# Optimization experiments

Hardware: AMD Instinct MI355X
Metric: run time of the kernel (lower is better)

The kernel has to match this reference:

```python
import jax, jax.numpy as jnp
import numpy as np

B = 2; C = 3; IMG = 224; P = 16
DIM = 256; DEPTH = 2; HEADS = 4; DH = 64; MLP = 1024; NCLS = 1000
GRID = IMG // P            # 14
NPATCH = GRID * GRID       # 196
T = NPATCH + 1             # 197 (cls token)
PATCH_DIM = C * P * P      # 768


def _ln(x, g, b):
    m = x.mean(-1, keepdims=True)
    v = ((x - m) ** 2).mean(-1, keepdims=True)
    return (x - m) * jax.lax.rsqrt(v + 1e-5) * g + b


def _trittention(x, ln_g, ln_b, w_abcde, b_abcde, w_out, b_out):
    b, t, _ = x.shape
    xn = _ln(x, ln_g, ln_b)
    abcde = xn @ w_abcde + b_abcde                      # [b,t,5*H*DH]
    a, bb, c, d, e = jnp.split(abcde, 5, axis=-1)
    rs = lambda z: z.reshape(b, t, HEADS, DH)
    a, bb, c, d, e = map(rs, (a, bb, c, d, e))
    # cubic ternary scores: [b, h, q, s, t]
    s = jnp.einsum('bshd,bthd,bqhd->bhqst', a, bb, c) / DH
    p = jax.nn.softmax(s.reshape(b, HEADS, t, t * t), axis=-1)
    p = p.reshape(b, HEADS, t, t, t)
    z = jnp.einsum('bhqlr,blhd->bhqd', p, d) + jnp.einsum('bhqlr,brhd->bhqd', p, e)
    z = z.transpose(0, 2, 1, 3).reshape(b, t, HEADS * DH)
    return z @ w_out + b_out


def _ff(x, ln_g, ln_b, w1, b1, w2, b2):
    h = jax.nn.gelu(_ln(x, ln_g, ln_b) @ w1 + b1, approximate=False)
    return h @ w2 + b2


def setup_inputs() -> dict:
    key = jax.random.key(0)
    ks = jax.random.split(key, 10)
    s = 0.02
    d = {}
    d['img'] = jax.random.normal(ks[0], (B, C, IMG, IMG), jnp.float32)
    d['patch_ln1_g'] = jnp.ones((PATCH_DIM,), jnp.float32)
    d['patch_ln1_b'] = jnp.zeros((PATCH_DIM,), jnp.float32)
    d['patch_w'] = jax.random.normal(ks[1], (PATCH_DIM, DIM), jnp.float32) * s
    d['patch_b'] = jnp.zeros((DIM,), jnp.float32)
    d['patch_ln2_g'] = jnp.ones((DIM,), jnp.float32)
    d['patch_ln2_b'] = jnp.zeros((DIM,), jnp.float32)
    d['pos_emb'] = jax.random.normal(ks[2], (1, T, DIM), jnp.float32) * s
    d['cls_token'] = jax.random.normal(ks[3], (1, 1, DIM), jnp.float32) * s
    d['attn_ln_g'] = jnp.ones((DEPTH, DIM), jnp.float32)
    d['attn_ln_b'] = jnp.zeros((DEPTH, DIM), jnp.float32)
    d['w_abcde'] = jax.random.normal(ks[4], (DEPTH, DIM, 5 * HEADS * DH), jnp.float32) * s
    d['b_abcde'] = jnp.zeros((DEPTH, 5 * HEADS * DH), jnp.float32)
    d['w_out'] = jax.random.normal(ks[5], (DEPTH, HEADS * DH, DIM), jnp.float32) * s
    d['b_out'] = jnp.zeros((DEPTH, DIM), jnp.float32)
    d['ff_ln_g'] = jnp.ones((DEPTH, DIM), jnp.float32)
    d['ff_ln_b'] = jnp.zeros((DEPTH, DIM), jnp.float32)
    d['ff_w1'] = jax.random.normal(ks[6], (DEPTH, DIM, MLP), jnp.float32) * s
    d['ff_b1'] = jnp.zeros((DEPTH, MLP), jnp.float32)
    d['ff_w2'] = jax.random.normal(ks[7], (DEPTH, MLP, DIM), jnp.float32) * s
    d['ff_b2'] = jnp.zeros((DEPTH, DIM), jnp.float32)
    d['final_ln_g'] = jnp.ones((DIM,), jnp.float32)
    d['final_ln_b'] = jnp.zeros((DIM,), jnp.float32)
    d['head_w'] = jax.random.normal(ks[8], (DIM, NCLS), jnp.float32) * s
    d['head_b'] = jnp.zeros((NCLS,), jnp.float32)
    return d


def reference(img, patch_ln1_g, patch_ln1_b, patch_w, patch_b, patch_ln2_g, patch_ln2_b,
              pos_emb, cls_token, attn_ln_g, attn_ln_b, w_abcde, b_abcde, w_out, b_out,
              ff_ln_g, ff_ln_b, ff_w1, ff_b1, ff_w2, ff_b2, final_ln_g, final_ln_b,
              head_w, head_b):
    b = img.shape[0]
    # Rearrange 'b c (h p1) (w p2) -> b (h w) (p1 p2 c)'
    x = img.reshape(b, C, GRID, P, GRID, P).transpose(0, 2, 4, 3, 5, 1)
    x = x.reshape(b, NPATCH, PATCH_DIM)
    x = _ln(x, patch_ln1_g, patch_ln1_b)
    x = x @ patch_w + patch_b
    x = _ln(x, patch_ln2_g, patch_ln2_b)
    cls = jnp.broadcast_to(cls_token, (b, 1, DIM))
    x = jnp.concatenate([cls, x], axis=1) + pos_emb
    for i in range(DEPTH):
        x = _trittention(x, attn_ln_g[i], attn_ln_b[i], w_abcde[i], b_abcde[i],
                         w_out[i], b_out[i]) + x
        x = _ff(x, ff_ln_g[i], ff_ln_b[i], ff_w1[i], ff_b1[i], ff_w2[i], ff_b2[i]) + x
    x = _ln(x, final_ln_g, final_ln_b)
    return x[:, 0] @ head_w + head_b
```

## Files before the change

kernel.cpp:

```cpp
#include <hip/hip_runtime.h>
#include <hip/hip_bf16.h>

#define BB 2
#define TT 197
#define TP 208
#define NT16 13
#define DIMM 256
#define HEADS_ 4
#define DH_ 64
#define ABCDE_N 1280
#define MLP_ 1024
#define NCLS_ 1000
#define PATCH_DIM_ 768

typedef __attribute__((ext_vector_type(8))) short short8_t;
typedef __attribute__((ext_vector_type(4))) float f32x4;

__device__ __forceinline__ float waveReduceSum(float v) {
#pragma unroll
    for (int off = 32; off > 0; off >>= 1) v += __shfl_xor(v, off, 64);
    return v;
}

__device__ __forceinline__ float rowReduceSum16(float v) {
    v += __uint_as_float(__builtin_amdgcn_update_dpp(
            0, __float_as_uint(v), 0x121, 0xF, 0xF, true));
    v += __uint_as_float(__builtin_amdgcn_update_dpp(
            0, __float_as_uint(v), 0x122, 0xF, 0xF, true));
    v += __uint_as_float(__builtin_amdgcn_update_dpp(
            0, __float_as_uint(v), 0x124, 0xF, 0xF, true));
    v += __uint_as_float(__builtin_amdgcn_update_dpp(
            0, __float_as_uint(v), 0x128, 0xF, 0xF, true));
    return v;
}

__device__ __forceinline__ unsigned short f2bf(float x) {
    unsigned int u = __float_as_uint(x);
    u += 0x7FFFu + ((u >> 16) & 1u);
    return (unsigned short)(u >> 16);
}

__device__ __forceinline__ float bf2f(unsigned short u) {
    return __uint_as_float(((unsigned int)u) << 16);
}

__global__ __launch_bounds__(256) void patch_embed_k(
    const float* __restrict__ img, const float* __restrict__ g1, const float* __restrict__ b1,
    const float* __restrict__ pw, const float* __restrict__ pb,
    const float* __restrict__ g2, const float* __restrict__ b2,
    const float* __restrict__ pos, const float* __restrict__ cls,
    float* __restrict__ xa)
{
    int tid = threadIdx.x;
    if (blockIdx.x == 98) {
        for (int b = 0; b < BB; b++)
            xa[(long)b * TT * DIMM + tid] = cls[tid] + pos[tid];
        return;
    }
    __shared__ __align__(16) float xs[4][PATCH_DIM_];
    __shared__ float red[8];
    int pr0 = blockIdx.x * 4;
    for (int r = 0; r < 4; r++) {
        int pr = pr0 + r;
        int b = pr / 196, patch = pr % 196;
        int gh = patch / 14, gw = patch % 14;
        for (int j = tid; j < PATCH_DIM_; j += 256) {
            int c = j % 3, p2 = (j / 3) % 16, p1 = j / 48;
            xs[r][j] = img[(((long)b * 3 + c) * 224 + gh * 16 + p1) * 224 + gw * 16 + p2];
        }
    }
    __syncthreads();
    int wv = tid >> 6, lane = tid & 63;
    {
        int r = wv;
        float s = 0.f, s2 = 0.f;
        for (int j = lane; j < PATCH_DIM_; j += 64) { float v = xs[r][j]; s += v; s2 += v * v; }
        s = waveReduceSum(s); s2 = waveReduceSum(s2);
        float m = s / PATCH_DIM_;
        float rs = rsqrtf(s2 / PATCH_DIM_ - m * m + 1e-5f);
        for (int j = lane; j < PATCH_DIM_; j += 64)
            xs[r][j] = (xs[r][j] - m) * rs * g1[j] + b1[j];
    }
    __syncthreads();
    float acc[4] = {0.f, 0.f, 0.f, 0.f};
    for (int k = 0; k < PATCH_DIM_; k += 4) {
        float w0 = pw[(k + 0) * DIMM + tid];
        float w1 = pw[(k + 1) * DIMM + tid];
        float w2 = pw[(k + 2) * DIMM + tid];
        float w3 = pw[(k + 3) * DIMM + tid];
#pragma unroll
        for (int r = 0; r < 4; r++) {
            float4 xv = *(const float4*)&xs[r][k];
            acc[r] = fmaf(xv.x, w0, fmaf(xv.y, w1, fmaf(xv.z, w2, fmaf(xv.w, w3, acc[r]))));
        }
    }
#pragma unroll
    for (int r = 0; r < 4; r++) acc[r] += pb[tid];
    for (int r = 0; r < 4; r++) {
        float s = waveReduceSum(acc[r]);
        float s2 = waveReduceSum(acc[r] * acc[r]);
        if (lane == 0) { red[wv * 2] = s; red[wv * 2 + 1] = s2; }
        __syncthreads();
        float S = red[0] + red[2] + red[4] + red[6];
        float S2 = red[1] + red[3] + red[5] + red[7];
        __syncthreads();
        float m = S / DIMM;
        float rs = rsqrtf(S2 / DIMM - m * m + 1e-5f);
        int pr = pr0 + r;
        int b = pr / 196, patch = pr % 196;
        float v = (acc[r] - m) * rs * g2[tid] + b2[tid] + pos[(1 + patch) * DIMM + tid];
        xa[((long)b * TT + 1 + patch) * DIMM + tid] = v;
    }
}

__global__ __launch_bounds__(512) void gemm_ksplit_k(
    const float* __restrict__ x, long x_stride, int M, int K, int N,
    const float* __restrict__ w, const float* __restrict__ bias,
    const float* __restrict__ res, float* __restrict__ out,
    const float* __restrict__ ln_g, const float* __restrict__ ln_b,
    int do_gelu)
{
    __shared__ __align__(16) float xs[4 * 1024];
    __shared__ float psum[8 * 4 * 64];
    int tid = threadIdx.x, lane = tid & 63, wv = tid >> 6;
    int row0 = blockIdx.y * 4, col0 = blockIdx.x * 64;

    for (int i = tid; i < 4 * K; i += 512) {
        int r = i / K, k = i - r * K;
        int row = row0 + r;
        xs[i] = (row < M) ? x[(long)row * x_stride + k] : 0.f;
    }
    __syncthreads();
    if (ln_g) {
        if (wv < 4) {
            float* xr = xs + wv * K;
            float s = 0.f, s2 = 0.f;
            for (int k = lane; k < K; k += 64) { float v = xr[k]; s += v; s2 += v * v; }
            s = waveReduceSum(s); s2 = waveReduceSum(s2);
            float m = s / K;
            float rs = rsqrtf(s2 / K - m * m + 1e-5f);
            for (int k = lane; k < K; k += 64)
                xr[k] = (xr[k] - m) * rs * ln_g[k] + ln_b[k];
        }
        __syncthreads();
    }

    int col = col0 + lane;
    float a0 = 0.f, a1 = 0.f, a2 = 0.f, a3 = 0.f;
    int kq = K >> 3;
    if (col < N) {
        const float* x0 = xs + wv * kq;
        const float* x1 = x0 + K;
        const float* x2 = x1 + K;
        const float* x3 = x2 + K;
        const float* wp = w + (long)(wv * kq) * N + col;
        long nl = N;
        for (int kk = 0; kk < kq; kk += 4) {
            float w0 = wp[0], w1 = wp[nl], w2 = wp[2 * nl], w3 = wp[3 * nl];
            wp += 4 * nl;
            float4 v0 = *(const float4*)(x0 + kk);
            float4 v1 = *(const float4*)(x1 + kk);
            float4 v2 = *(const float4*)(x2 + kk);
            float4 v3 = *(const float4*)(x3 + kk);
            a0 = fmaf(v0.x, w0, fmaf(v0.y, w1, fmaf(v0.z, w2, fmaf(v0.w, w3, a0))));
            a1 = fmaf(v1.x, w0, fmaf(v1.y, w1, fmaf(v1.z, w2, fmaf(v1.w, w3, a1))));
            a2 = fmaf(v2.x, w0, fmaf(v2.y, w1, fmaf(v2.z, w2, fmaf(v2.w, w3, a2))));
            a3 = fmaf(v3.x, w0, fmaf(v3.y, w1, fmaf(v3.z, w2, fmaf(v3.w, w3, a3))));
        }
    }
    psum[wv * 256 + 0 * 64 + lane] = a0;
    psum[wv * 256 + 1 * 64 + lane] = a1;
    psum[wv * 256 + 2 * 64 + lane] = a2;
    psum[wv * 256 + 3 * 64 + lane] = a3;
    __syncthreads();

    if (tid < 256) {
        int r = tid >> 6, c = tid & 63;
        float v = ((psum[r * 64 + c]        + psum[256 + r * 64 + c])
                +  (psum[512 + r * 64 + c]  + psum[768 + r * 64 + c]))
                + ((psum[1024 + r * 64 + c] + psum[1280 + r * 64 + c])
                +  (psum[1536 + r * 64 + c] + psum[1792 + r * 64 + c]));
        int row = row0 + r, cw = col0 + c;
        if (row < M && cw < N) {
            if (bias) v += bias[cw];
            if (do_gelu) v = 0.5f * v * (1.f + erff(v * 0.70710678118654752f));
            if (res) v += res[(long)row * N + cw];
            out[(long)row * N + cw] = v;
        }
    }
}

__global__ __launch_bounds__(256) void tritt_k(
    const float* __restrict__ abcde, float* __restrict__ z)
{
    __shared__ __align__(16) unsigned short a_lds[TP * 64];
    __shared__ __align__(16) unsigned short b_lds[TP * 64];
    __shared__ float pl_s[4][TP];
    __shared__ float pr_s[4][TP];

    int tid = threadIdx.x, lane = tid & 63, wv = tid >> 6;
    int bh = blockIdx.y;
    int b = bh >> 2, h = bh & 3;
    const float* base = abcde + (long)b * TT * ABCDE_N;
    const float SC = 1.4426950408889634f / 64.f;

    for (int i = tid; i < TP * 8; i += 256) {
        int row = i >> 3, ch = i & 7;
        int idx = row * 64 + ((ch * 8) ^ ((row & 7) << 3));
        unsigned short av[8], bv[8];
        if (row < TT) {
            const float* srcA = base + (long)row * ABCDE_N + h * 64 + ch * 8;
            const float* srcB = srcA + 256;
            float4 a0 = *(const float4*)(srcA);
            float4 a1 = *(const float4*)(srcA + 4);
            float4 b0 = *(const float4*)(srcB);
            float4 b1 = *(const float4*)(srcB + 4);
            av[0] = f2bf(a0.x); av[1] = f2bf(a0.y); av[2] = f2bf(a0.z); av[3] = f2bf(a0.w);
            av[4] = f2bf(a1.x); av[5] = f2bf(a1.y); av[6] = f2bf(a1.z); av[7] = f2bf(a1.w);
            bv[0] = f2bf(b0.x); bv[1] = f2bf(b0.y); bv[2] = f2bf(b0.z); bv[3] = f2bf(b0.w);
            bv[4] = f2bf(b1.x); bv[5] = f2bf(b1.y); bv[6] = f2bf(b1.z); bv[7] = f2bf(b1.w);
        } else {
#pragma unroll
            for (int j = 0; j < 8; j++) { av[j] = 0; bv[j] = 0; }
        }
        *(short8_t*)&a_lds[idx] = *(const short8_t*)av;
        *(short8_t*)&b_lds[idx] = *(const short8_t*)bv;
    }
    __syncthreads();

    int q = blockIdx.x * 4 + wv;
    if (q >= TT) return;

    int lm = lane & 15;
    int lg = lane >> 4;

    const float* cp = base + (long)q * ABCDE_N + 512 + h * 64;
    float c0[8], c1[8];
    {
        float4 v0 = *(const float4*)(cp + lg * 8);
        float4 v1 = *(const float4*)(cp + lg * 8 + 4);
        float4 v2 = *(const float4*)(cp + (lg + 4) * 8);
        float4 v3 = *(const float4*)(cp + (lg + 4) * 8 + 4);
        c0[0] = v0.x * SC; c0[1] = v0.y * SC; c0[2] = v0.z * SC; c0[3] = v0.w * SC;
        c0[4] = v1.x * SC; c0[5] = v1.y * SC; c0[6] = v1.z * SC; c0[7] = v1.w * SC;
        c1[0] = v2.x * SC; c1[1] = v2.y * SC; c1[2] = v2.z * SC; c1[3] = v2.w * SC;
        c1[4] = v3.x * SC; c1[5] = v3.y * SC; c1[6] = v3.z * SC; c1[7] = v3.w * SC;
    }

    short8_t bf0[NT16], bf1[NT16];
#pragma unroll
    for (int j = 0; j < NT16; j++) {
        int brow = j * 16 + lm;
        bf0[j] = *(const short8_t*)&b_lds[brow * 64 + (((lg    ) * 8) ^ ((brow & 7) << 3))];
        bf1[j] = *(const short8_t*)&b_lds[brow * 64 + (((lg + 4) * 8) ^ ((brow & 7) << 3))];
    }

    float pcol[NT16];
#pragma unroll
    for (int j = 0; j < NT16; j++) pcol[j] = 0.f;

#pragma unroll 1
    for (int i = 0; i < NT16; i++) {
        int arow = i * 16 + lm;
        short8_t af0 = *(const short8_t*)&a_lds[arow * 64 + (((lg    ) * 8) ^ ((arow & 7) << 3))];
        short8_t af1 = *(const short8_t*)&a_lds[arow * 64 + (((lg + 4) * 8) ^ ((arow & 7) << 3))];
        short8_t ac0, ac1;
#pragma unroll
        for (int e = 0; e < 8; e++) {
            ac0[e] = (short)f2bf(bf2f((unsigned short)af0[e]) * c0[e]);
            ac1[e] = (short)f2bf(bf2f((unsigned short)af1[e]) * c1[e]);
        }
        float prow[4] = {0.f, 0.f, 0.f, 0.f};
#pragma unroll
        for (int j = 0; j < NT16; j++) {
            f32x4 acc = {0.f, 0.f, 0.f, 0.f};
            acc = __builtin_amdgcn_mfma_f32_16x16x32_bf16(ac0, bf0[j], acc, 0, 0, 0);
            acc = __builtin_amdgcn_mfma_f32_16x16x32_bf16(ac1, bf1[j], acc, 0, 0, 0);
            float e0 = __builtin_amdgcn_exp2f(acc[0]);
            float e1 = __builtin_amdgcn_exp2f(acc[1]);
            float e2 = __builtin_amdgcn_exp2f(acc[2]);
            float e3 = __builtin_amdgcn_exp2f(acc[3]);
            prow[0] += e0; prow[1] += e1; prow[2] += e2; prow[3] += e3;
            pcol[j] += (e0 + e1) + (e2 + e3);
        }
#pragma unroll
        for (int r = 0; r < 4; r++) prow[r] = rowReduceSum16(prow[r]);
        if (lm == 0) {
            int rb = i * 16 + lg * 4;
#pragma unroll
            for (int r = 0; r < 4; r++) pl_s[wv][rb + r] = prow[r];
        }
    }
#pragma unroll
    for (int j = 0; j < NT16; j++) {
        float c = pcol[j];
        c += __shfl_xor(c, 16, 64);
        c += __shfl_xor(c, 32, 64);
        if (lane < 16) pr_s[wv][j * 16 + lane] = c;
    }

    float zpart = 0.f;
    for (int s = lane; s < TT; s += 64) zpart += pl_s[wv][s];
    zpart = waveReduceSum(zpart);
    float rz = 1.f / (zpart - 11.f * TT);

    const float* dp = base + 768 + h * 64 + lane;
    const float* ep = base + 1024 + h * 64 + lane;
    float z0 = 0.f, z1 = 0.f, z2 = 0.f, z3 = 0.f;
    int s = 0;
    for (; s + 1 < TT; s += 2) {
        z0 = fmaf(pl_s[wv][s]     - 11.f, dp[(long)s * ABCDE_N],       z0);
        z1 = fmaf(pr_s[wv][s]     - 11.f, ep[(long)s * ABCDE_N],       z1);
        z2 = fmaf(pl_s[wv][s + 1] - 11.f, dp[(long)(s + 1) * ABCDE_N], z2);
        z3 = fmaf(pr_s[wv][s + 1] - 11.f, ep[(long)(s + 1) * ABCDE_N], z3);
    }
    z0 = fmaf(pl_s[wv][s] - 11.f, dp[(long)s * ABCDE_N], z0);
    z1 = fmaf(pr_s[wv][s] - 11.f, ep[(long)s * ABCDE_N], z1);
    z[((long)b * TT + q) * DIMM + h * 64 + lane] = ((z0 + z1) + (z2 + z3)) * rz;
}

extern "C" void kernel_launch(void* const* d_in, const int* in_sizes, int n_in,
                              void* d_out, int out_size, void* d_ws, size_t ws_size,
                              hipStream_t stream)
{
    const float* img    = (const float*)d_in[0];
    const float* g1     = (const float*)d_in[1];
    const float* b1     = (const float*)d_in[2];
    const float* pw     = (const float*)d_in[3];
    const float* pb     = (const float*)d_in[4];
    const float* g2     = (const float*)d_in[5];
    const float* b2     = (const float*)d_in[6];
    const float* pos    = (const float*)d_in[7];
    const float* cls    = (const float*)d_in[8];
    const float* attn_g = (const float*)d_in[9];
    const float* attn_b = (const float*)d_in[10];
    const float* w_abc  = (const float*)d_in[11];
    const float* b_abc  = (const float*)d_in[12];
    const float* w_out  = (const float*)d_in[13];
    const float* b_out  = (const float*)d_in[14];
    const float* ff_g   = (const float*)d_in[15];
    const float* ff_b   = (const float*)d_in[16];
    const float* w1     = (const float*)d_in[17];
    const float* b1f    = (const float*)d_in[18];
    const float* w2     = (const float*)d_in[19];
    const float* b2f    = (const float*)d_in[20];
    const float* fin_g  = (const float*)d_in[21];
    const float* fin_b  = (const float*)d_in[22];
    const float* hw     = (const float*)d_in[23];
    const float* hb     = (const float*)d_in[24];
    float* out = (float*)d_out;

    const int MROWS = BB * TT;
    float* ws = (float*)d_ws;
    float* xa = ws;
    float* xb = xa + (long)MROWS * DIMM;
    float* zb = xb + (long)MROWS * DIMM;
    float* ab = zb + (long)MROWS * DIMM;

    patch_embed_k<<<99, 256, 0, stream>>>(img, g1, b1, pw, pb, g2, b2, pos, cls, xa);

    const int GY = (MROWS + 3) / 4;
    const int QT4 = (TT + 3) / 4;
    for (int i = 0; i < 2; i++) {
        gemm_ksplit_k<<<dim3(ABCDE_N / 64, GY), 512, 0, stream>>>(
            xa, DIMM, MROWS, DIMM, ABCDE_N,
            w_abc + (long)i * DIMM * ABCDE_N, b_abc + (long)i * ABCDE_N,
            nullptr, ab, attn_g + i * DIMM, attn_b + i * DIMM, 0);
        tritt_k<<<dim3(QT4, BB * HEADS_), 256, 0, stream>>>(ab, zb);
        gemm_ksplit_k<<<dim3(DIMM / 64, GY), 512, 0, stream>>>(
            zb, DIMM, MROWS, DIMM, DIMM,
            w_out + (long)i * DIMM * DIMM, b_out + (long)i * DIMM,
            xa, xb, nullptr, nullptr, 0);
        gemm_ksplit_k<<<dim3(MLP_ / 64, GY), 512, 0, stream>>>(
            xb, DIMM, MROWS, DIMM, MLP_,
            w1 + (long)i * DIMM * MLP_, b1f + (long)i * MLP_,
            nullptr, ab, ff_g + i * DIMM, ff_b + i * DIMM, 1);
        gemm_ksplit_k<<<dim3(DIMM / 64, GY), 512, 0, stream>>>(
            ab, MLP_, MROWS, MLP_, DIMM,
            w2 + (long)i * MLP_ * DIMM, b2f + (long)i * DIMM,
            xb, xa, nullptr, nullptr, 0);
    }
    gemm_ksplit_k<<<dim3((NCLS_ + 63) / 64, 1), 512, 0, stream>>>(
        xa, (long)TT * DIMM, BB, DIMM, NCLS_,
        hw, hb, nullptr, out, fin_g, fin_b, 0);
}
```

Before: 223.7 us.

## Split patch-embed K across 1024 threads and prefetch next A fragment in tritt

Patch embedding now runs 1024 threads per block, splitting the 768-long reduction into four K-slices whose partial sums are combined through shared memory before the LayerNorm. This raises parallelism in a kernel that launches only 99 blocks. The trittention inner loop also software-pipelines the LDS loads of the next A row-tile while the current tile's MFMAs and exponentials run. The costs are extra shared memory, an extra barrier, idle threads during the reductions, and more register pressure in the tritt loop.

```diff
diff --git a/kernel.cpp b/kernel.cpp
--- a/kernel.cpp
+++ b/kernel.cpp
@@ -44,7 +44,7 @@
     return __uint_as_float(((unsigned int)u) << 16);
 }
 
-__global__ __launch_bounds__(256) void patch_embed_k(
+__global__ __launch_bounds__(1024) void patch_embed_k(
     const float* __restrict__ img, const float* __restrict__ g1, const float* __restrict__ b1,
     const float* __restrict__ pw, const float* __restrict__ pb,
     const float* __restrict__ g2, const float* __restrict__ b2,
@@ -53,26 +53,28 @@
 {
     int tid = threadIdx.x;
     if (blockIdx.x == 98) {
-        for (int b = 0; b < BB; b++)
-            xa[(long)b * TT * DIMM + tid] = cls[tid] + pos[tid];
+        if (tid < DIMM)
+            for (int b = 0; b < BB; b++)
+                xa[(long)b * TT * DIMM + tid] = cls[tid] + pos[tid];
         return;
     }
     __shared__ __align__(16) float xs[4][PATCH_DIM_];
+    __shared__ float psum[4][4][DIMM];
     __shared__ float red[8];
     int pr0 = blockIdx.x * 4;
-    for (int r = 0; r < 4; r++) {
+    int wv16 = tid >> 6, lane = tid & 63;
+
+    for (int i = tid; i < 4 * PATCH_DIM_; i += 1024) {
+        int r = i / PATCH_DIM_, j = i - r * PATCH_DIM_;
         int pr = pr0 + r;
         int b = pr / 196, patch = pr % 196;
         int gh = patch / 14, gw = patch % 14;
-        for (int j = tid; j < PATCH_DIM_; j += 256) {
-            int c = j % 3, p2 = (j / 3) % 16, p1 = j / 48;
-            xs[r][j] = img[(((long)b * 3 + c) * 224 + gh * 16 + p1) * 224 + gw * 16 + p2];
-        }
-    }
-    __syncthreads();
-    int wv = tid >> 6, lane = tid & 63;
-    {
-        int r = wv;
+        int c = j % 3, p2 = (j / 3) % 16, p1 = j / 48;
+        xs[r][j] = img[(((long)b * 3 + c) * 224 + gh * 16 + p1) * 224 + gw * 16 + p2];
+    }
+    __syncthreads();
+    if (wv16 < 4) {
+        int r = wv16;
         float s = 0.f, s2 = 0.f;
         for (int j = lane; j < PATCH_DIM_; j += 64) { float v = xs[r][j]; s += v; s2 += v * v; }
         s = waveReduceSum(s); s2 = waveReduceSum(s2);
@@ -82,12 +84,14 @@
             xs[r][j] = (xs[r][j] - m) * rs * g1[j] + b1[j];
     }
     __syncthreads();
+    int col = tid & 255, ks = tid >> 8;
+    int k0 = ks * (PATCH_DIM_ / 4);
     float acc[4] = {0.f, 0.f, 0.f, 0.f};
-    for (int k = 0; k < PATCH_DIM_; k += 4) {
-        float w0 = pw[(k + 0) * DIMM + tid];
-        float w1 = pw[(k + 1) * DIMM + tid];
-        float w2 = pw[(k + 2) * DIMM + tid];
-        float w3 = pw[(k + 3) * DIMM + tid];
+    for (int k = k0; k < k0 + PATCH_DIM_ / 4; k += 4) {
+        float w0 = pw[(k + 0) * DIMM + col];
+        float w1 = pw[(k + 1) * DIMM + col];
+        float w2 = pw[(k + 2) * DIMM + col];
+        float w3 = pw[(k + 3) * DIMM + col];
 #pragma unroll
         for (int r = 0; r < 4; r++) {
             float4 xv = *(const float4*)&xs[r][k];
@@ -95,21 +99,35 @@
         }
     }
 #pragma unroll
-    for (int r = 0; r < 4; r++) acc[r] += pb[tid];
+    for (int r = 0; r < 4; r++) psum[ks][r][col] = acc[r];
+    __syncthreads();
+
+    float v4[4];
+    if (tid < 256) {
+#pragma unroll
+        for (int r = 0; r < 4; r++)
+            v4[r] = (psum[0][r][tid] + psum[1][r][tid])
+                  + (psum[2][r][tid] + psum[3][r][tid]) + pb[tid];
+    }
     for (int r = 0; r < 4; r++) {
-        float s = waveReduceSum(acc[r]);
-        float s2 = waveReduceSum(acc[r] * acc[r]);
-        if (lane == 0) { red[wv * 2] = s; red[wv * 2 + 1] = s2; }
+        float s = 0.f, s2 = 0.f;
+        if (tid < 256) {
+            s = waveReduceSum(v4[r]);
+            s2 = waveReduceSum(v4[r] * v4[r]);
+            if (lane == 0) { red[wv16 * 2] = s; red[wv16 * 2 + 1] = s2; }
+        }
         __syncthreads();
         float S = red[0] + red[2] + red[4] + red[6];
         float S2 = red[1] + red[3] + red[5] + red[7];
         __syncthreads();
-        float m = S / DIMM;
-        float rs = rsqrtf(S2 / DIMM - m * m + 1e-5f);
-        int pr = pr0 + r;
-        int b = pr / 196, patch = pr % 196;
-        float v = (acc[r] - m) * rs * g2[tid] + b2[tid] + pos[(1 + patch) * DIMM + tid];
-        xa[((long)b * TT + 1 + patch) * DIMM + tid] = v;
+        if (tid < 256) {
+            float m = S / DIMM;
+            float rs = rsqrtf(S2 / DIMM - m * m + 1e-5f);
+            int pr = pr0 + r;
+            int b = pr / 196, patch = pr % 196;
+            float v = (v4[r] - m) * rs * g2[tid] + b2[tid] + pos[(1 + patch) * DIMM + tid];
+            xa[((long)b * TT + 1 + patch) * DIMM + tid] = v;
+        }
     }
 }
 
@@ -259,11 +277,18 @@
 #pragma unroll
     for (int j = 0; j < NT16; j++) pcol[j] = 0.f;
 
+    int arow = lm;
+    short8_t af0 = *(const short8_t*)&a_lds[arow * 64 + (((lg    ) * 8) ^ ((arow & 7) << 3))];
+    short8_t af1 = *(const short8_t*)&a_lds[arow * 64 + (((lg + 4) * 8) ^ ((arow & 7) << 3))];
+
 #pragma unroll 1
     for (int i = 0; i < NT16; i++) {
-        int arow = i * 16 + lm;
-        short8_t af0 = *(const short8_t*)&a_lds[arow * 64 + (((lg    ) * 8) ^ ((arow & 7) << 3))];
-        short8_t af1 = *(const short8_t*)&a_lds[arow * 64 + (((lg + 4) * 8) ^ ((arow & 7) << 3))];
+        short8_t nf0 = af0, nf1 = af1;
+        if (i + 1 < NT16) {
+            int nrow = (i + 1) * 16 + lm;
+            nf0 = *(const short8_t*)&a_lds[nrow * 64 + (((lg    ) * 8) ^ ((nrow & 7) << 3))];
+            nf1 = *(const short8_t*)&a_lds[nrow * 64 + (((lg + 4) * 8) ^ ((nrow & 7) << 3))];
+        }
         short8_t ac0, ac1;
 #pragma unroll
         for (int e = 0; e < 8; e++) {
@@ -290,6 +315,7 @@
 #pragma unroll
             for (int r = 0; r < 4; r++) pl_s[wv][rb + r] = prow[r];
         }
+        af0 = nf0; af1 = nf1;
     }
 #pragma unroll
     for (int j = 0; j < NT16; j++) {
@@ -357,7 +383,7 @@
     float* zb = xb + (long)MROWS * DIMM;
     float* ab = zb + (long)MROWS * DIMM;
 
-    patch_embed_k<<<99, 256, 0, stream>>>(img, g1, b1, pw, pb, g2, b2, pos, cls, xa);
+    patch_embed_k<<<99, 1024, 0, stream>>>(img, g1, b1, pw, pb, g2, b2, pos, cls, xa);
 
     const int GY = (MROWS + 3) / 4;
     const int QT4 = (TT + 3) / 4;
```

New measurement: 211.2 us. 1.06x faster.
